# Optimization experiments

Measured on AMD Instinct MI355X. Metric: run time of the kernel, lower is better.

The kernel has to match this reference:

```python
import jax, jax.numpy as jnp
import numpy as np

B, S, D, H = 4, 1024, 512, 8
EPS = 1e-5


def _cx(x):
    # [..., 2] float -> complex
    return jax.lax.complex(x[..., 0], x[..., 1])


def setup_inputs() -> dict:
    key = jax.random.key(0)
    ks = jax.random.split(key, 9)
    f = lambda k, sh: jax.random.normal(k, sh, dtype=jnp.float32)
    inp = {
        "q": f(ks[0], (B, S, D, 2)),
        "k": f(ks[1], (B, S, D, 2)),
        "v": f(ks[2], (B, S, D, 2)),
        "Wq": f(ks[3], (D, D, 2)) * 0.02,
        "bq": f(ks[4], (D, 2)) * 0.02,
        "Wk": f(ks[5], (D, D, 2)) * 0.02,
        "bk": f(ks[6], (D, 2)) * 0.02,
        "Wv": f(ks[7], (D, D, 2)) * 0.02,
        "bv": f(ks[8], (D, 2)) * 0.02,
        "gamma_r": jnp.ones((D,), jnp.float32),
        "beta_r": jnp.zeros((D,), jnp.float32),
        "gamma_i": jnp.ones((D,), jnp.float32),
        "beta_i": jnp.zeros((D,), jnp.float32),
        "n_heads": H,
    }
    return inp


def _layernorm(x, g, b):
    # torch LayerNorm: biased variance, eps inside sqrt
    mu = jnp.mean(x, axis=-1, keepdims=True)
    var = jnp.mean((x - mu) ** 2, axis=-1, keepdims=True)
    return (x - mu) / jnp.sqrt(var + EPS) * g + b


def reference(q, k, v, Wq, bq, Wk, bk, Wv, bv, gamma_r, beta_r, gamma_i, beta_i, n_heads):
    qc, kc, vc = _cx(q), _cx(k), _cx(v)
    # complex linear: x @ W^T + b
    Q = jnp.einsum("bsd,ed->bse", qc, _cx(Wq)) + _cx(bq)
    K = jnp.einsum("bsd,ed->bse", kc, _cx(Wk)) + _cx(bk)
    V = jnp.einsum("bsd,ed->bse", vc, _cx(Wv)) + _cx(bv)
    b, s, d = qc.shape
    dh = d // n_heads
    Qh = Q.reshape(b, s, n_heads, dh)
    Kh = K.reshape(b, s, n_heads, dh)
    Vh = V.reshape(b, s, n_heads, dh)
    # complex scores [b,h,q,k], scaled by sqrt(dh)
    scores = jnp.einsum("bqhd,bkhd->bhqk", Qh, Kh) / jnp.sqrt(jnp.float32(dh))
    # original: softmax over view_as_real dim=-2 == key axis, real & imag independently
    attn = jax.lax.complex(jax.nn.softmax(scores.real, axis=-1),
                           jax.nn.softmax(scores.imag, axis=-1))
    # (dropout is identity in eval mode)
    out = jnp.einsum("bhqk,bkhd->bqhd", attn, Vh).reshape(b, s, d)
    out = out + qc  # residual
    out_r = _layernorm(out.real, gamma_r, beta_r)
    out_i = _layernorm(out.imag, gamma_i, beta_i)
    return jnp.stack([out_r, out_i], axis=-1)  # [B,S,D,2]
```

## Files before the change

kernel.cpp:

```cpp
#include <hip/hip_runtime.h>
#include <math.h>

#define BB  4
#define SS  1024
#define DD  512
#define HH  8
#define DHD 64
#define PL  2097152
#define WPL 262144

constexpr float LN_EPS = 1e-5f;

using half4 = __attribute__((ext_vector_type(4))) _Float16;
using half8 = __attribute__((ext_vector_type(8))) _Float16;
using f32x4 = __attribute__((ext_vector_type(4))) float;

__device__ __forceinline__ half8 negh(half8 a) {
    union { half8 h; unsigned int u[4]; } t;
    t.h = a;
    #pragma unroll
    for (int i = 0; i < 4; ++i) t.u[i] ^= 0x80008000u;
    return t.h;
}
__device__ __forceinline__ half8 ldh64(const unsigned short* p, int row, int col) {
    return *(const half8*)(p + row * 64 + (col ^ ((row & 7) << 3)));
}
#define MFMA16(acc, a, b) acc = __builtin_amdgcn_mfma_f32_16x16x32_f16(a, b, acc, 0, 0, 0)

__global__ __launch_bounds__(256)
void cvt_kernel(const float2* __restrict__ s0, const float2* __restrict__ s1,
                const float2* __restrict__ s2, unsigned short* __restrict__ dst,
                int planeElems) {
    const int z = blockIdx.y;
    const float2* src = z == 0 ? s0 : (z == 1 ? s1 : s2);
    unsigned short* base = dst + (size_t)z * 2 * planeElems;
    const int idx = (blockIdx.x * 256 + threadIdx.x) * 2;
    float4 t = *(const float4*)(src + idx);
    union { _Float16 h[2]; unsigned int u; } r, i;
    r.h[0] = (_Float16)t.x; r.h[1] = (_Float16)t.z;
    i.h[0] = (_Float16)t.y; i.h[1] = (_Float16)t.w;
    ((unsigned int*)(base))[idx >> 1] = r.u;
    ((unsigned int*)(base + planeElems))[idx >> 1] = i.u;
}

__global__ __launch_bounds__(256, 5)
void proj_kernel(const unsigned short* __restrict__ XP,
                 const unsigned short* __restrict__ WP,
                 const float2* __restrict__ bq, const float2* __restrict__ bk,
                 const float2* __restrict__ bv,
                 unsigned short* __restrict__ QG, unsigned short* __restrict__ KG,
                 unsigned short* __restrict__ VG) {
    const unsigned short* XR = XP + (size_t)blockIdx.z * 2 * PL;
    const unsigned short* XI = XR + PL;
    const unsigned short* WR = WP + (size_t)blockIdx.z * 2 * WPL;
    const unsigned short* WI = WR + WPL;
    const float2* bias; unsigned short* outP;
    if (blockIdx.z == 0)      { bias = bq; outP = QG; }
    else if (blockIdx.z == 1) { bias = bk; outP = KG; }
    else                      { bias = bv; outP = VG; }
    const bool isV = (blockIdx.z == 2);

    __shared__ unsigned short Xs[2][4096];
    __shared__ unsigned short Ws[2][4096];

    const int tid  = threadIdx.x;
    const int w    = tid >> 6;
    const int lane = tid & 63;
    const int quad = lane >> 4;
    const int l15  = lane & 15;
    const int m0   = blockIdx.x * 64;
    const int h    = blockIdx.y;
    const int e0   = h * 64;

    const int r8 = tid >> 3;
    const int g8 = tid & 7;

    f32x4 Sr[4], Si[4];
    #pragma unroll
    for (int i = 0; i < 4; ++i) { Sr[i] = (f32x4)0.f; Si[i] = (f32x4)0.f; }

    for (int dc = 0; dc < DD; dc += 64) {
        if (dc) __syncthreads();
        #pragma unroll
        for (int it = 0; it < 2; ++it) {
            const int row = it * 32 + r8;
            const int off = row * 64 + ((g8 ^ (row & 7)) << 3);
            const size_t xo = (size_t)(m0 + row) * DD + dc + g8 * 8;
            const size_t wo = (size_t)(e0 + row) * DD + dc + g8 * 8;
            *(uint4*)&Xs[0][off] = *(const uint4*)(XR + xo);
            *(uint4*)&Xs[1][off] = *(const uint4*)(XI + xo);
            *(uint4*)&Ws[0][off] = *(const uint4*)(WR + wo);
            *(uint4*)&Ws[1][off] = *(const uint4*)(WI + wo);
        }
        __syncthreads();

        const int mrow = w * 16 + l15;
        #pragma unroll
        for (int kc = 0; kc < 2; ++kc) {
            const int dl = kc * 32 + quad * 8;
            half8 xr  = ldh64(Xs[0], mrow, dl);
            half8 xi  = ldh64(Xs[1], mrow, dl);
            half8 xmi = negh(xi);
            #pragma unroll
            for (int et = 0; et < 4; ++et) {
                const int er = et * 16 + l15;
                half8 wr = ldh64(Ws[0], er, dl);
                half8 wi = ldh64(Ws[1], er, dl);
                MFMA16(Sr[et], xr,  wr);
                MFMA16(Sr[et], xmi, wi);
                MFMA16(Si[et], xr,  wi);
                MFMA16(Si[et], xi,  wr);
            }
        }
    }

    #pragma unroll
    for (int et = 0; et < 4; ++et) {
        const int col = et * 16 + l15;
        float2 bb = bias[e0 + col];
        #pragma unroll
        for (int reg = 0; reg < 4; ++reg) {
            int m = m0 + w * 16 + quad * 4 + reg;
            int b = m >> 10;
            int s = m & 1023;
            int bh = b * HH + h;
            union { _Float16 h; unsigned short u; } cr, ci;
            cr.h = (_Float16)(Sr[et][reg] + bb.x);
            ci.h = (_Float16)(Si[et][reg] + bb.y);
            size_t o = isV ? ((size_t)bh * DHD + col) * SS + s
                           : ((size_t)bh * SS + s) * DHD + col;
            outP[0 * PL + o] = cr.u;
            outP[1 * PL + o] = ci.u;
        }
    }
}

#define AWID 72
__global__ __launch_bounds__(256, 2)
void attn_kernel(const unsigned short* __restrict__ QG, const unsigned short* __restrict__ KG,
                 const unsigned short* __restrict__ VG,
                 unsigned short* __restrict__ ObR, unsigned short* __restrict__ ObI) {
    __shared__ unsigned short Ks[2][64 * AWID];
    __shared__ unsigned short Vt[2][64 * AWID];
    __shared__ unsigned short Ps[2][64 * AWID];
    __shared__ float lbuf[2][2][64];

    const int n   = blockIdx.x;
    const int bh  = (n & 7) * 4 + (n >> 7);
    const int q0  = ((n >> 3) & 15) * 64;
    const int b   = bh >> 3;
    const int h   = bh & 7;

    const int tid  = threadIdx.x;
    const int w    = tid >> 6;
    const int lane = tid & 63;
    const int quad = lane >> 4;
    const int l15  = lane & 15;
    const int sw   = w & 1;
    const int tw   = w >> 1;

    half8 qfr[2][2], qfi[2][2], qfmi[2][2];
    #pragma unroll
    for (int qt = 0; qt < 2; ++qt)
        #pragma unroll
        for (int kc = 0; kc < 2; ++kc) {
            size_t qa = ((size_t)bh * SS + q0 + sw * 32 + qt * 16 + l15) * DHD + kc * 32 + quad * 8;
            qfr[qt][kc]  = *(const half8*)(QG + qa);
            qfi[qt][kc]  = *(const half8*)(QG + PL + qa);
            qfmi[qt][kc] = negh(qfi[qt][kc]);
        }

    f32x4 acc[2][2][4];
    #pragma unroll
    for (int qt = 0; qt < 2; ++qt)
        #pragma unroll
        for (int dt = 0; dt < 2; ++dt)
            #pragma unroll
            for (int p = 0; p < 4; ++p) acc[qt][dt][p] = (f32x4)0.f;
    float lacc[2][2] = {{0.f, 0.f}, {0.f, 0.f}};

    const int srow = tid >> 3;
    const int sg   = (tid & 7) * 8;

    for (int kt = 0; kt < SS; kt += 64) {
        __syncthreads();
        #pragma unroll
        for (int p = 0; p < 2; ++p)
            #pragma unroll
            for (int it = 0; it < 2; ++it) {
                const int r = it * 32 + srow;
                *(uint4*)&Ks[p][r * AWID + sg] =
                    *(const uint4*)(KG + (size_t)p * PL + ((size_t)bh * SS + kt + r) * DHD + sg);
                *(uint4*)&Vt[p][r * AWID + sg] =
                    *(const uint4*)(VG + (size_t)p * PL + ((size_t)bh * DHD + r) * SS + kt + sg);
            }
        __syncthreads();

        f32x4 Sr[2][2], Si[2][2];
        #pragma unroll
        for (int a = 0; a < 2; ++a)
            #pragma unroll
            for (int c = 0; c < 2; ++c) { Sr[a][c] = (f32x4)0.f; Si[a][c] = (f32x4)0.f; }
        #pragma unroll
        for (int kc = 0; kc < 2; ++kc) {
            #pragma unroll
            for (int kt2 = 0; kt2 < 2; ++kt2) {
                const int krow = tw * 32 + kt2 * 16 + l15;
                half8 akr = *(const half8*)&Ks[0][krow * AWID + kc * 32 + quad * 8];
                half8 aki = *(const half8*)&Ks[1][krow * AWID + kc * 32 + quad * 8];
                #pragma unroll
                for (int qt = 0; qt < 2; ++qt) {
                    MFMA16(Sr[kt2][qt], akr, qfr[qt][kc]);
                    MFMA16(Sr[kt2][qt], aki, qfmi[qt][kc]);
                    MFMA16(Si[kt2][qt], aki, qfr[qt][kc]);
                    MFMA16(Si[kt2][qt], akr, qfi[qt][kc]);
                }
            }
        }

        #pragma unroll
        for (int kt2 = 0; kt2 < 2; ++kt2)
            #pragma unroll
            for (int qt = 0; qt < 2; ++qt) {
                half4 pr, pi;
                float sr_ = 0.f, si_ = 0.f;
                #pragma unroll
                for (int reg = 0; reg < 4; ++reg) {
                    float er = __expf(Sr[kt2][qt][reg] * 0.125f);
                    float ei = __expf(Si[kt2][qt][reg] * 0.125f);
                    pr[reg] = (_Float16)er;
                    pi[reg] = (_Float16)ei;
                    sr_ += (float)pr[reg];
                    si_ += (float)pi[reg];
                }
                lacc[qt][0] += sr_;
                lacc[qt][1] += si_;
                const int qrow = sw * 32 + qt * 16 + l15;
                const int kcol = tw * 32 + kt2 * 16 + quad * 4;
                *(half4*)&Ps[0][qrow * AWID + kcol] = pr;
                *(half4*)&Ps[1][qrow * AWID + kcol] = pi;
            }
        __syncthreads();

        #pragma unroll
        for (int kc = 0; kc < 2; ++kc) {
            half8 ap[2][2];
            #pragma unroll
            for (int qt = 0; qt < 2; ++qt) {
                const int qrow = sw * 32 + qt * 16 + l15;
                ap[qt][0] = *(const half8*)&Ps[0][qrow * AWID + kc * 32 + quad * 8];
                ap[qt][1] = *(const half8*)&Ps[1][qrow * AWID + kc * 32 + quad * 8];
            }
            #pragma unroll
            for (int dt = 0; dt < 2; ++dt) {
                const int drow = tw * 32 + dt * 16 + l15;
                half8 bvr = *(const half8*)&Vt[0][drow * AWID + kc * 32 + quad * 8];
                half8 bvi = *(const half8*)&Vt[1][drow * AWID + kc * 32 + quad * 8];
                #pragma unroll
                for (int qt = 0; qt < 2; ++qt) {
                    MFMA16(acc[qt][dt][0], ap[qt][0], bvr);
                    MFMA16(acc[qt][dt][1], ap[qt][0], bvi);
                    MFMA16(acc[qt][dt][2], ap[qt][1], bvr);
                    MFMA16(acc[qt][dt][3], ap[qt][1], bvi);
                }
            }
        }
    }

    __syncthreads();
    #pragma unroll
    for (int qt = 0; qt < 2; ++qt)
        #pragma unroll
        for (int p = 0; p < 2; ++p) {
            float v = lacc[qt][p];
            v += __shfl_xor(v, 16);
            v += __shfl_xor(v, 32);
            if (lane < 16) lbuf[p][tw][sw * 32 + qt * 16 + lane] = v;
        }
    __syncthreads();

    #pragma unroll
    for (int qt = 0; qt < 2; ++qt)
        #pragma unroll
        for (int reg = 0; reg < 4; ++reg) {
            const int qloc = sw * 32 + qt * 16 + quad * 4 + reg;
            const float ir = 1.f / (lbuf[0][0][qloc] + lbuf[0][1][qloc]);
            const float ii = 1.f / (lbuf[1][0][qloc] + lbuf[1][1][qloc]);
            #pragma unroll
            for (int dt = 0; dt < 2; ++dt) {
                const int d = tw * 32 + dt * 16 + l15;
                union { _Float16 h; unsigned short u; } cr, ci;
                cr.h = (_Float16)(acc[qt][dt][0][reg] * ir - acc[qt][dt][3][reg] * ii);
                ci.h = (_Float16)(acc[qt][dt][1][reg] * ir + acc[qt][dt][2][reg] * ii);
                size_t o = ((size_t)b * SS + q0 + qloc) * DD + h * DHD + d;
                ObR[o] = cr.u;
                ObI[o] = ci.u;
            }
        }
}

__global__ __launch_bounds__(256)
void ln_kernel(const unsigned short* __restrict__ OrP, const unsigned short* __restrict__ OiP,
               const float2* __restrict__ Qin,
               const float* __restrict__ gr, const float* __restrict__ br,
               const float* __restrict__ gi, const float* __restrict__ bi,
               float2* __restrict__ out) {
    const int row = blockIdx.x;
    const int tid = threadIdx.x;
    const size_t base = (size_t)row * DD;
    const int e0 = 2 * tid, e1 = 2 * tid + 1;

    union { unsigned int u; _Float16 h[2]; } tr, ti;
    tr.u = *(const unsigned int*)(OrP + base + e0);
    ti.u = *(const unsigned int*)(OiP + base + e0);
    float2 r0 = Qin[base + e0];
    float2 r1 = Qin[base + e1];
    float xr0 = (float)tr.h[0] + r0.x;
    float xr1 = (float)tr.h[1] + r1.x;
    float xi0 = (float)ti.h[0] + r0.y;
    float xi1 = (float)ti.h[1] + r1.y;

    float sr = xr0 + xr1;
    float si = xi0 + xi1;
    float qr = xr0 * xr0 + xr1 * xr1;
    float qi = xi0 * xi0 + xi1 * xi1;
    #pragma unroll
    for (int off = 32; off > 0; off >>= 1) {
        sr += __shfl_down(sr, off);
        si += __shfl_down(si, off);
        qr += __shfl_down(qr, off);
        qi += __shfl_down(qi, off);
    }
    __shared__ float red[4][4];
    __shared__ float stat[4];
    int lane = tid & 63, wid = tid >> 6;
    if (lane == 0) { red[wid][0] = sr; red[wid][1] = si; red[wid][2] = qr; red[wid][3] = qi; }
    __syncthreads();
    if (tid == 0) {
        sr = red[0][0] + red[1][0] + red[2][0] + red[3][0];
        si = red[0][1] + red[1][1] + red[2][1] + red[3][1];
        qr = red[0][2] + red[1][2] + red[2][2] + red[3][2];
        qi = red[0][3] + red[1][3] + red[2][3] + red[3][3];
        float mur = sr * (1.f / DD), mui = si * (1.f / DD);
        float vr = qr * (1.f / DD) - mur * mur;
        float vi = qi * (1.f / DD) - mui * mui;
        stat[0] = mur; stat[1] = mui;
        stat[2] = rsqrtf(vr + LN_EPS); stat[3] = rsqrtf(vi + LN_EPS);
    }
    __syncthreads();
    float mur = stat[0], mui = stat[1], rsr = stat[2], rsi = stat[3];
    out[base + e0] = make_float2((xr0 - mur) * rsr * gr[e0] + br[e0],
                                 (xi0 - mui) * rsi * gi[e0] + bi[e0]);
    out[base + e1] = make_float2((xr1 - mur) * rsr * gr[e1] + br[e1],
                                 (xi1 - mui) * rsi * gi[e1] + bi[e1]);
}

extern "C" void kernel_launch(void* const* d_in, const int* in_sizes, int n_in,
                              void* d_out, int out_size, void* d_ws, size_t ws_size,
                              hipStream_t stream) {
    const float2* q  = (const float2*)d_in[0];
    const float2* k  = (const float2*)d_in[1];
    const float2* v  = (const float2*)d_in[2];
    const float2* Wq = (const float2*)d_in[3];
    const float2* bq = (const float2*)d_in[4];
    const float2* Wk = (const float2*)d_in[5];
    const float2* bk = (const float2*)d_in[6];
    const float2* Wv = (const float2*)d_in[7];
    const float2* bv = (const float2*)d_in[8];
    const float*  gr = (const float*)d_in[9];
    const float*  br = (const float*)d_in[10];
    const float*  gi = (const float*)d_in[11];
    const float*  bi = (const float*)d_in[12];

    unsigned short* XP  = (unsigned short*)d_ws;
    unsigned short* WP  = XP + (size_t)6 * PL;
    unsigned short* QG  = WP + (size_t)6 * WPL;
    unsigned short* KG  = QG + (size_t)2 * PL;
    unsigned short* VG  = KG + (size_t)2 * PL;
    unsigned short* ObR = VG + (size_t)2 * PL;
    unsigned short* ObI = ObR + (size_t)PL;

    cvt_kernel<<<dim3(4096, 3), 256, 0, stream>>>(q, k, v, XP, PL);
    cvt_kernel<<<dim3(512, 3), 256, 0, stream>>>(Wq, Wk, Wv, WP, WPL);
    proj_kernel<<<dim3(64, 8, 3), 256, 0, stream>>>(XP, WP, bq, bk, bv, QG, KG, VG);
    attn_kernel<<<dim3(512), 256, 0, stream>>>(QG, KG, VG, ObR, ObI);
    ln_kernel<<<dim3(BB * SS), 256, 0, stream>>>(ObR, ObI, q, gr, br, gi, bi, (float2*)d_out);
}
```

Before: 221.3 us.

## Enlarge projection GEMM tiles to 128x128 with async double-buffered LDS loads

The complex projection kernel moves from 64x64 output tiles to 128x128 tiles, with each wave computing a 64x64 sub-tile (4x4 MFMA fragments per real/imag part). Global-to-LDS staging uses global_load_lds in a double-buffered pipeline, so the next K-chunk loads while the current one is computed. The aim is higher operand reuse per LDS read and overlap of memory with MFMA work. In exchange the grid shrinks from 1536 to 384 blocks, occupancy drops to one block per CU with larger register and LDS use, and the output scatter is unchanged.

```diff
diff --git a/kernel.cpp b/kernel.cpp
--- a/kernel.cpp
+++ b/kernel.cpp
@@ -43,7 +43,7 @@
     ((unsigned int*)(base + planeElems))[idx >> 1] = i.u;
 }
 
-__global__ __launch_bounds__(256, 5)
+__global__ __launch_bounds__(256, 1)
 void proj_kernel(const unsigned short* __restrict__ XP,
                  const unsigned short* __restrict__ WP,
                  const float2* __restrict__ bq, const float2* __restrict__ bk,
@@ -52,85 +52,118 @@
                  unsigned short* __restrict__ VG) {
     const unsigned short* XR = XP + (size_t)blockIdx.z * 2 * PL;
     const unsigned short* XI = XR + PL;
-    const unsigned short* WR = WP + (size_t)blockIdx.z * 2 * WPL;
-    const unsigned short* WI = WR + WPL;
+    const unsigned short* WRp = WP + (size_t)blockIdx.z * 2 * WPL;
+    const unsigned short* WIp = WRp + WPL;
     const float2* bias; unsigned short* outP;
     if (blockIdx.z == 0)      { bias = bq; outP = QG; }
     else if (blockIdx.z == 1) { bias = bk; outP = KG; }
     else                      { bias = bv; outP = VG; }
     const bool isV = (blockIdx.z == 2);
 
-    __shared__ unsigned short Xs[2][4096];
-    __shared__ unsigned short Ws[2][4096];
+    __shared__ __align__(16) unsigned short Xs[2][2][128 * 64];
+    __shared__ __align__(16) unsigned short Ws[2][2][128 * 64];
 
     const int tid  = threadIdx.x;
     const int w    = tid >> 6;
     const int lane = tid & 63;
     const int quad = lane >> 4;
     const int l15  = lane & 15;
-    const int m0   = blockIdx.x * 64;
-    const int h    = blockIdx.y;
-    const int e0   = h * 64;
-
-    const int r8 = tid >> 3;
-    const int g8 = tid & 7;
-
-    f32x4 Sr[4], Si[4];
-    #pragma unroll
-    for (int i = 0; i < 4; ++i) { Sr[i] = (f32x4)0.f; Si[i] = (f32x4)0.f; }
-
-    for (int dc = 0; dc < DD; dc += 64) {
-        if (dc) __syncthreads();
-        #pragma unroll
-        for (int it = 0; it < 2; ++it) {
-            const int row = it * 32 + r8;
-            const int off = row * 64 + ((g8 ^ (row & 7)) << 3);
-            const size_t xo = (size_t)(m0 + row) * DD + dc + g8 * 8;
-            const size_t wo = (size_t)(e0 + row) * DD + dc + g8 * 8;
-            *(uint4*)&Xs[0][off] = *(const uint4*)(XR + xo);
-            *(uint4*)&Xs[1][off] = *(const uint4*)(XI + xo);
-            *(uint4*)&Ws[0][off] = *(const uint4*)(WR + wo);
-            *(uint4*)&Ws[1][off] = *(const uint4*)(WI + wo);
-        }
-        __syncthreads();
-
-        const int mrow = w * 16 + l15;
+    const int wm   = w >> 1;
+    const int we   = w & 1;
+    const int m0   = blockIdx.x * 128;
+    const int e0   = blockIdx.y * 128;
+
+    const int srow = lane >> 3;
+    const int sg   = lane & 7;
+    const int scol = ((sg ^ srow) << 3);
+    const unsigned short* gplane;
+    unsigned short* l0p; unsigned short* l1p;
+    int row0;
+    if (w == 0)      { gplane = XR;  row0 = m0; l0p = &Xs[0][0][0]; l1p = &Xs[1][0][0]; }
+    else if (w == 1) { gplane = XI;  row0 = m0; l0p = &Xs[0][1][0]; l1p = &Xs[1][1][0]; }
+    else if (w == 2) { gplane = WRp; row0 = e0; l0p = &Ws[0][0][0]; l1p = &Ws[1][0][0]; }
+    else             { gplane = WIp; row0 = e0; l0p = &Ws[0][1][0]; l1p = &Ws[1][1][0]; }
+    const unsigned short* gs = gplane + (size_t)(row0 + srow) * DD + scol;
+
+#define STAGE(LB, DC) { \
+        const unsigned short* _g = gs + (DC); \
+        _Pragma("unroll") \
+        for (int j = 0; j < 16; ++j) \
+            __builtin_amdgcn_global_load_lds( \
+                (const __attribute__((address_space(1))) void*)(_g + j * 8 * DD), \
+                (__attribute__((address_space(3))) void*)((LB) + j * 512), \
+                16, 0, 0); \
+    }
+
+    f32x4 Sr[4][4], Si[4][4];
+    #pragma unroll
+    for (int a = 0; a < 4; ++a)
+        #pragma unroll
+        for (int c = 0; c < 4; ++c) { Sr[a][c] = (f32x4)0.f; Si[a][c] = (f32x4)0.f; }
+
+    STAGE(l0p, 0);
+    __syncthreads();
+
+    #pragma unroll 2
+    for (int s = 0; s < 8; ++s) {
+        if (s < 7) STAGE(((s & 1) ? l0p : l1p), (s + 1) * 64);
+
+        const unsigned short* xb0 = &Xs[s & 1][0][0];
+        const unsigned short* xb1 = &Xs[s & 1][1][0];
+        const unsigned short* wb0 = &Ws[s & 1][0][0];
+        const unsigned short* wb1 = &Ws[s & 1][1][0];
+
         #pragma unroll
         for (int kc = 0; kc < 2; ++kc) {
             const int dl = kc * 32 + quad * 8;
-            half8 xr  = ldh64(Xs[0], mrow, dl);
-            half8 xi  = ldh64(Xs[1], mrow, dl);
-            half8 xmi = negh(xi);
-            #pragma unroll
-            for (int et = 0; et < 4; ++et) {
-                const int er = et * 16 + l15;
-                half8 wr = ldh64(Ws[0], er, dl);
-                half8 wi = ldh64(Ws[1], er, dl);
-                MFMA16(Sr[et], xr,  wr);
-                MFMA16(Sr[et], xmi, wi);
-                MFMA16(Si[et], xr,  wi);
-                MFMA16(Si[et], xi,  wr);
-            }
-        }
-    }
-
-    #pragma unroll
-    for (int et = 0; et < 4; ++et) {
-        const int col = et * 16 + l15;
-        float2 bb = bias[e0 + col];
-        #pragma unroll
-        for (int reg = 0; reg < 4; ++reg) {
-            int m = m0 + w * 16 + quad * 4 + reg;
-            int b = m >> 10;
-            int s = m & 1023;
-            int bh = b * HH + h;
-            union { _Float16 h; unsigned short u; } cr, ci;
-            cr.h = (_Float16)(Sr[et][reg] + bb.x);
-            ci.h = (_Float16)(Si[et][reg] + bb.y);
-            size_t o = isV ? ((size_t)bh * DHD + col) * SS + s
-                           : ((size_t)bh * SS + s) * DHD + col;
-            outP[0 * PL + o] = cr.u;
-            outP[1 * PL + o] = ci.u;
+            half8 xr[4], xi[4];
+            #pragma unroll
+            for (int mf = 0; mf < 4; ++mf) {
+                const int mr = wm * 64 + mf * 16 + l15;
+                xr[mf] = ldh64(xb0, mr, dl);
+                xi[mf] = ldh64(xb1, mr, dl);
+            }
+            #pragma unroll
+            for (int ef = 0; ef < 4; ++ef) {
+                const int er = we * 64 + ef * 16 + l15;
+                half8 wr  = ldh64(wb0, er, dl);
+                half8 wi  = ldh64(wb1, er, dl);
+                half8 wmi = negh(wi);
+                #pragma unroll
+                for (int mf = 0; mf < 4; ++mf) {
+                    MFMA16(Sr[mf][ef], xr[mf], wr);
+                    MFMA16(Sr[mf][ef], xi[mf], wmi);
+                    MFMA16(Si[mf][ef], xr[mf], wi);
+                    MFMA16(Si[mf][ef], xi[mf], wr);
+                }
+            }
+        }
+        __syncthreads();
+    }
+#undef STAGE
+
+    #pragma unroll
+    for (int ef = 0; ef < 4; ++ef) {
+        const int eg  = e0 + we * 64 + ef * 16 + l15;
+        const int hh  = eg >> 6;
+        const int col = eg & 63;
+        float2 bb = bias[eg];
+        #pragma unroll
+        for (int mf = 0; mf < 4; ++mf) {
+            #pragma unroll
+            for (int reg = 0; reg < 4; ++reg) {
+                int m = m0 + wm * 64 + mf * 16 + quad * 4 + reg;
+                int bidx = m >> 10;
+                int sidx = m & 1023;
+                int bh = bidx * HH + hh;
+                union { _Float16 h; unsigned short u; } cr, ci;
+                cr.h = (_Float16)(Sr[mf][ef][reg] + bb.x);
+                ci.h = (_Float16)(Si[mf][ef][reg] + bb.y);
+                size_t o = isV ? ((size_t)bh * DHD + col) * SS + sidx
+                               : ((size_t)bh * SS + sidx) * DHD + col;
+                outP[0 * PL + o] = cr.u;
+                outP[1 * PL + o] = ci.u;
+            }
         }
     }
 }
@@ -382,7 +415,7 @@
 
     cvt_kernel<<<dim3(4096, 3), 256, 0, stream>>>(q, k, v, XP, PL);
     cvt_kernel<<<dim3(512, 3), 256, 0, stream>>>(Wq, Wk, Wv, WP, WPL);
-    proj_kernel<<<dim3(64, 8, 3), 256, 0, stream>>>(XP, WP, bq, bk, bv, QG, KG, VG);
+    proj_kernel<<<dim3(32, 4, 3), 256, 0, stream>>>(XP, WP, bq, bk, bv, QG, KG, VG);
     attn_kernel<<<dim3(512), 256, 0, stream>>>(QG, KG, VG, ObR, ObI);
     ln_kernel<<<dim3(BB * SS), 256, 0, stream>>>(ObR, ObI, q, gr, br, gi, bi, (float2*)d_out);
 }
```

After: 216.7 us. -2.1%, faster.
